# Kernel optimization log

Measured on AMD Instinct MI355X. Metric: run time of the kernel, lower is better.

## Reference

```python
import jax, jax.numpy as jnp
import numpy as np

NUM_HEADS = 16
LN_EPS = 1e-5


def setup_inputs() -> dict:
    key = jax.random.key(0)
    k1, k2, k3 = jax.random.split(key, 3)
    E = 1024
    B, S = 4, 2048
    return {
        "rotation_params": jax.random.normal(k1, (E, E), dtype=jnp.float32) * (E ** -0.5),
        "entangle_params": jax.random.normal(k2, (E, E), dtype=jnp.float32) * (E ** -0.5),
        "inputs": jax.random.normal(k3, (B, S, E), dtype=jnp.float32),
        "ln_weight": jnp.ones((E,), dtype=jnp.float32),
        "ln_bias": jnp.zeros((E,), dtype=jnp.float32),
    }


def reference(rotation_params, entangle_params, inputs, ln_weight, ln_bias):
    x = inputs  # (B, S, E)
    B, S, E = x.shape
    H = NUM_HEADS
    D = E // H
    scale = D ** -0.5

    q = jnp.einsum('bse,ef->bsf', x, rotation_params)
    k = jnp.einsum('bse,ef->bsf', x, entangle_params)
    v = x  # forward uses raw inputs as values

    # split heads: (B, H, S, D)
    q = q.reshape(B, S, H, D).transpose(0, 2, 1, 3)
    k = k.reshape(B, S, H, D).transpose(0, 2, 1, 3)
    v = v.reshape(B, S, H, D).transpose(0, 2, 1, 3)

    scores = jnp.einsum('bhsd,bhtd->bhst', q, k) * scale  # (B, H, S, S)
    attn = jax.nn.softmax(scores, axis=-1)
    context = jnp.einsum('bhst,bhtd->bhsd', attn, v)
    context = context.transpose(0, 2, 1, 3).reshape(B, S, E)

    # residual + LayerNorm
    y = context + x
    mu = jnp.mean(y, axis=-1, keepdims=True)
    var = jnp.mean(jnp.square(y - mu), axis=-1, keepdims=True)
    y = (y - mu) * jax.lax.rsqrt(var + LN_EPS)
    return y * ln_weight + ln_bias
```

## Files before the change

kernel.cpp:

```cpp
#include <hip/hip_runtime.h>
#include <hip/hip_bf16.h>

#define LOG2E 1.44269504088896340736f

typedef __attribute__((ext_vector_type(8)))  short  short8;
typedef __attribute__((ext_vector_type(2)))  float  f32x2;
typedef __attribute__((ext_vector_type(4)))  float  f32x4;
typedef __attribute__((ext_vector_type(16))) float  f32x16;

__device__ __forceinline__ unsigned short f2bf(float f) {
  unsigned u = __builtin_bit_cast(unsigned, f);
  return (unsigned short)((u + 0x8000u) >> 16);
}
__device__ __forceinline__ float bf2f(unsigned short u) {
  return __builtin_bit_cast(float, (unsigned)u << 16);
}
__device__ __forceinline__ f32x2 pkadd(f32x2 a, f32x2 b) {
  f32x2 r; asm("v_pk_add_f32 %0, %1, %2" : "=v"(r) : "v"(a), "v"(b)); return r;
}
__device__ __forceinline__ unsigned cvtpk2(float a, float b) {
  unsigned r; asm("v_cvt_pk_bf16_f32 %0, %1, %2" : "=v"(r) : "v"(a), "v"(b)); return r;
}
__device__ __forceinline__ float hexp2(float x) {
  float r; asm("v_exp_f32 %0, %1" : "=v"(r) : "v"(x)); return r;
}
__device__ __forceinline__ float m3(float a, float b, float c) {
  return fmaxf(fmaxf(a, b), c);
}
__device__ __forceinline__ void gl16(const void* g, void* l) {
  __builtin_amdgcn_global_load_lds(
      (const __attribute__((address_space(1))) void*)g,
      (__attribute__((address_space(3))) void*)l, 16, 0, 0);
}


__global__ __launch_bounds__(256) void prep_wt(const float* __restrict__ R,
                                               const float* __restrict__ En,
                                               unsigned short* __restrict__ Rt,
                                               unsigned short* __restrict__ Et) {
  const float* src = blockIdx.z ? En : R;
  unsigned short* dst = blockIdx.z ? Et : Rt;
  __shared__ unsigned short t[64][65];
  int e0 = blockIdx.y * 64, f0 = blockIdx.x * 64;
  int tid = threadIdx.x;
  int r = tid >> 2, c4 = (tid & 3) * 16;
#pragma unroll
  for (int j = 0; j < 16; j += 4) {
    float4 v = *(const float4*)(src + (size_t)(e0 + r) * 1024 + f0 + c4 + j);
    t[c4 + j + 0][r] = f2bf(v.x);
    t[c4 + j + 1][r] = f2bf(v.y);
    t[c4 + j + 2][r] = f2bf(v.z);
    t[c4 + j + 3][r] = f2bf(v.w);
  }
  __syncthreads();
  short8 o0, o1;
#pragma unroll
  for (int j = 0; j < 8; j++) {
    o0[j] = (short)t[r][c4 + j];
    o1[j] = (short)t[r][c4 + 8 + j];
  }
  *(short8*)(dst + (size_t)(f0 + r) * 1024 + e0 + c4) = o0;
  *(short8*)(dst + (size_t)(f0 + r) * 1024 + e0 + c4 + 8) = o1;
}

__global__ __launch_bounds__(256) void prep_vt(const float* __restrict__ x,
                                               unsigned short* __restrict__ vt,
                                               unsigned short* __restrict__ xb) {
  int bh = blockIdx.y, b = bh >> 4, h = bh & 15;
  int s0 = blockIdx.x * 64;
  __shared__ unsigned short t[64][65];
  int tid = threadIdx.x;
  int r = tid >> 2, c4 = (tid & 3) * 16;
#pragma unroll
  for (int j = 0; j < 16; j += 4) {
    float4 v = *(const float4*)(x + (size_t)(b * 2048 + s0 + r) * 1024 + h * 64 + c4 + j);
    ushort4 o;
    o.x = f2bf(v.x); o.y = f2bf(v.y); o.z = f2bf(v.z); o.w = f2bf(v.w);
    t[c4 + j + 0][r] = o.x;
    t[c4 + j + 1][r] = o.y;
    t[c4 + j + 2][r] = o.z;
    t[c4 + j + 3][r] = o.w;
    *(ushort4*)(xb + (size_t)(b * 2048 + s0 + r) * 1024 + h * 64 + c4 + j) = o;
  }
  __syncthreads();
  short8 o0, o1;
#pragma unroll
  for (int j = 0; j < 8; j++) {
    o0[j] = (short)t[r][c4 + j];
    o1[j] = (short)t[r][c4 + 8 + j];
  }
  *(short8*)(vt + (size_t)(bh * 64 + r) * 2048 + s0 + c4) = o0;
  *(short8*)(vt + (size_t)(bh * 64 + r) * 2048 + s0 + c4 + 8) = o1;
}

__global__ __launch_bounds__(256) void gemm_qk2(const unsigned short* __restrict__ A,
                                                const unsigned short* __restrict__ Bw,
                                                unsigned short* __restrict__ qb,
                                                unsigned short* __restrict__ kb,
                                                float qs) {
  int m0 = blockIdx.x * 128, n0 = blockIdx.y * 128;
  int tid = threadIdx.x;
  int w = tid >> 6, l = tid & 63;
  int wr = w >> 1, wc = w & 1;
  int l15 = l & 15, lq = l >> 4;

  __shared__ unsigned short As[128 * 64];
  __shared__ unsigned short Bs[128 * 64];

  f32x4 acc[4][4] = {};

  for (int k0 = 0; k0 < 1024; k0 += 64) {
    __syncthreads();
#pragma unroll
    for (int i = 0; i < 4; i++) {
      int row = i * 32 + (tid >> 3), ch = tid & 7;
      gl16(A  + (size_t)(m0 + row) * 1024 + k0 + ((ch ^ (row & 7)) << 3),
           (char*)As + i * 4096 + w * 1024);
      gl16(Bw + (size_t)(n0 + row) * 1024 + k0 + ((ch ^ (row & 7)) << 3),
           (char*)Bs + i * 4096 + w * 1024);
    }
    __syncthreads();

    short8 af[4][2], bfr[4][2];
#pragma unroll
    for (int mf = 0; mf < 4; mf++)
#pragma unroll
      for (int kk = 0; kk < 2; kk++) {
        int row = wr * 64 + mf * 16 + l15;
        int kb2 = (kk * 32 + lq * 8) * 2;
        af[mf][kk] = *(const short8*)((const char*)As + row * 128 + (kb2 ^ ((row & 7) << 4)));
      }
#pragma unroll
    for (int nf = 0; nf < 4; nf++)
#pragma unroll
      for (int kk = 0; kk < 2; kk++) {
        int row = wc * 64 + nf * 16 + l15;
        int kb2 = (kk * 32 + lq * 8) * 2;
        bfr[nf][kk] = *(const short8*)((const char*)Bs + row * 128 + (kb2 ^ ((row & 7) << 4)));
      }
#pragma unroll
    for (int mf = 0; mf < 4; mf++)
#pragma unroll
      for (int nf = 0; nf < 4; nf++)
#pragma unroll
        for (int kk = 0; kk < 2; kk++)
          acc[mf][nf] = __builtin_amdgcn_mfma_f32_16x16x32_bf16(
              af[mf][kk], bfr[nf][kk], acc[mf][nf], 0, 0, 0);
  }

  unsigned short* out = (n0 < 1024) ? qb : kb;
  float scale = (n0 < 1024) ? qs : 1.0f;
  int cb = n0 & 1023;
#pragma unroll
  for (int mf = 0; mf < 4; mf++)
#pragma unroll
    for (int nf = 0; nf < 4; nf++)
#pragma unroll
      for (int r = 0; r < 4; r++) {
        int grow = m0 + wr * 64 + mf * 16 + lq * 4 + r;
        int gcol = cb + wc * 64 + nf * 16 + l15;
        out[(size_t)grow * 1024 + gcol] = f2bf(acc[mf][nf][r] * scale);
      }
}

__global__ __launch_bounds__(256, 4) void attn_k(const unsigned short* __restrict__ Q,
                                                 const unsigned short* __restrict__ K,
                                                 const unsigned short* __restrict__ VT,
                                                 unsigned short* __restrict__ ctx) {
  int f = blockIdx.x;
  int bh = ((f >> 7) << 3) | (f & 7);
  int qt = (f >> 3) & 15;
  int b = bh >> 4, h = bh & 15;
  int q0 = qt * 128;
  int tid = threadIdx.x;
  int w = tid >> 6, l = tid & 63;
  int lh = l >> 5, l31 = l & 31;

  __shared__ unsigned short Kl[2 * 64 * 64];
  __shared__ unsigned short Vl[2 * 64 * 64];

  int qrow = q0 + w * 32 + l31;
  const unsigned short* qp = Q + (size_t)(b * 2048 + qrow) * 1024 + h * 64;
  short8 qf[4];
#pragma unroll
  for (int dk = 0; dk < 4; dk++) qf[dk] = *(const short8*)(qp + dk * 16 + lh * 8);

  int key = (l31 & 7) << 4;
  int koff[4], voff[4];
#pragma unroll
  for (int dk = 0; dk < 4; dk++) koff[dk] = l31 * 128 + ((dk * 32 + lh * 16) ^ key);
#pragma unroll
  for (int tf = 0; tf < 2; tf++)
#pragma unroll
    for (int kk = 0; kk < 2; kk++)
      voff[tf * 2 + kk] = l31 * 128 + ((tf * 64 + kk * 32 + lh * 16) ^ key);

  const char* KB = (const char*)Kl;
  const char* VB = (const char*)Vl;

  f32x16 cacc[2] = {};
  float mrun = -INFINITY, lsl = 0.f;

#define STAGE(buf, tt)                                                        \
  {                                                                           \
    _Pragma("unroll") for (int i_ = 0; i_ < 2; i_++) {                        \
      int row_ = i_ * 32 + (tid >> 3), ch_ = tid & 7;                         \
      gl16(K + (size_t)(b * 2048 + (tt) + row_) * 1024 + h * 64 +             \
               ((ch_ ^ (row_ & 7)) << 3),                                     \
           (char*)Kl + (buf) * 8192 + i_ * 4096 + w * 1024);                  \
      gl16(VT + (size_t)(bh * 64 + row_) * 2048 + (tt) +                      \
               ((ch_ ^ (row_ & 7)) << 3),                                     \
           (char*)Vl + (buf) * 8192 + i_ * 4096 + w * 1024);                  \
    }                                                                         \
  }

#define COMPUTE(IMM)                                                          \
  do {                                                                        \
    f32x16 sacc[2] = {};                                                      \
    __builtin_amdgcn_s_setprio(1);                                            \
    _Pragma("unroll") for (int tf = 0; tf < 2; tf++)                          \
      _Pragma("unroll") for (int dk = 0; dk < 4; dk++) {                      \
        short8 kf = *(const short8*)(KB + koff[dk] + (IMM) + tf * 4096);      \
        sacc[tf] = __builtin_amdgcn_mfma_f32_32x32x16_bf16(kf, qf[dk],        \
                                                           sacc[tf], 0, 0, 0);\
      }                                                                       \
    __builtin_amdgcn_s_setprio(0);                                            \
    float t16[16];                                                            \
    _Pragma("unroll") for (int j = 0; j < 16; j++)                            \
      t16[j] = fmaxf(sacc[0][j], sacc[1][j]);                                 \
    float t8[8];                                                              \
    _Pragma("unroll") for (int j = 0; j < 8; j++)                             \
      t8[j] = fmaxf(t16[j], t16[j + 8]);                                      \
    float lmax = m3(m3(t8[0], t8[1], t8[2]), m3(t8[3], t8[4], t8[5]),         \
                    fmaxf(t8[6], t8[7]));                                     \
    if (!__all(lmax <= mrun + 8.f)) {                                         \
      unsigned lu = __builtin_bit_cast(unsigned, lmax);                       \
      auto rr = __builtin_amdgcn_permlane32_swap(lu, lu, false, false);       \
      float pm = fmaxf(__builtin_bit_cast(float, rr[0]),                      \
                       __builtin_bit_cast(float, rr[1]));                     \
      float mnew = fmaxf(mrun, pm);                                           \
      float alpha = hexp2(mrun - mnew);                                       \
      mrun = mnew; lsl *= alpha;                                              \
      _Pragma("unroll") for (int r = 0; r < 16; r++) {                        \
        int rowq = (r & 3) + ((r >> 2) << 3) + (lh << 2);                     \
        float ar = __shfl(alpha, rowq, 64);                                   \
        cacc[0][r] *= ar; cacc[1][r] *= ar;                                   \
      }                                                                       \
    }                                                                         \
    f32x2 negm2; negm2[0] = -mrun; negm2[1] = -mrun;                          \
    f32x2 r2; r2[0] = 0.f; r2[1] = 0.f;                                       \
    _Pragma("unroll") for (int tf = 0; tf < 2; tf++) {                        \
      unsigned pw[8];                                                         \
      _Pragma("unroll") for (int j = 0; j < 8; j++) {                         \
        f32x2 s2; s2[0] = sacc[tf][2 * j]; s2[1] = sacc[tf][2 * j + 1];       \
        f32x2 d = pkadd(s2, negm2);                                           \
        float e0 = hexp2(d[0]), e1 = hexp2(d[1]);                             \
        f32x2 e2; e2[0] = e0; e2[1] = e1;                                     \
        r2 = pkadd(r2, e2);                                                   \
        pw[j] = cvtpk2(e0, e1);                                               \
      }                                                                       \
      short8 pa[2];                                                           \
      _Pragma("unroll") for (int kk = 0; kk < 2; kk++) {                      \
        auto r02 = __builtin_amdgcn_permlane32_swap(pw[kk * 4 + 0],           \
                                                    pw[kk * 4 + 2], false, false); \
        auto r13 = __builtin_amdgcn_permlane32_swap(pw[kk * 4 + 1],           \
                                                    pw[kk * 4 + 3], false, false); \
        union { unsigned u[4]; short8 s8; } wv;                               \
        wv.u[0] = r02[0]; wv.u[1] = r13[0];                                   \
        wv.u[2] = r02[1]; wv.u[3] = r13[1];                                   \
        pa[kk] = wv.s8;                                                       \
      }                                                                       \
      __builtin_amdgcn_s_setprio(1);                                          \
      _Pragma("unroll") for (int kk = 0; kk < 2; kk++)                        \
        _Pragma("unroll") for (int df = 0; df < 2; df++) {                    \
          short8 vf = *(const short8*)(VB + voff[tf * 2 + kk] + (IMM) +       \
                                       df * 4096);                            \
          cacc[df] = __builtin_amdgcn_mfma_f32_32x32x16_bf16(pa[kk], vf,      \
                                                             cacc[df], 0, 0, 0); \
        }                                                                     \
      __builtin_amdgcn_s_setprio(0);                                          \
    }                                                                         \
    lsl += r2[0] + r2[1];                                                     \
  } while (0)

  STAGE(0, 0);
  __syncthreads();

  for (int tc2 = 0; tc2 < 16; tc2++) {
    int t0 = tc2 * 128;
    STAGE(1, t0 + 64);
    COMPUTE(0);
    __syncthreads();
    if (tc2 < 15) STAGE(0, t0 + 128);
    COMPUTE(8192);
    __syncthreads();
  }
#undef STAGE
#undef COMPUTE

  {
    unsigned lu = __builtin_bit_cast(unsigned, lsl);
    auto rr = __builtin_amdgcn_permlane32_swap(lu, lu, false, false);
    lsl = __builtin_bit_cast(float, rr[0]) + __builtin_bit_cast(float, rr[1]);
  }
  float linv = 1.f / lsl;
#pragma unroll
  for (int r = 0; r < 16; r++) {
    int rowq = (r & 3) + ((r >> 2) << 3) + (lh << 2);
    float lr = __shfl(linv, rowq, 64);
    size_t base = (size_t)(b * 2048 + q0 + w * 32 + rowq) * 1024 + h * 64 + l31;
    ctx[base]      = f2bf(cacc[0][r] * lr);
    ctx[base + 32] = f2bf(cacc[1][r] * lr);
  }
}

__global__ __launch_bounds__(256) void ln_k(const unsigned short* __restrict__ ctx,
                                            const float* __restrict__ x,
                                            const float* __restrict__ wgt,
                                            const float* __restrict__ bgam,
                                            float* __restrict__ out) {
  int row = blockIdx.x;
  int tid = threadIdx.x;
  size_t base = (size_t)row * 1024 + tid * 4;
  ushort4 cu = *(const ushort4*)(ctx + base);
  float4 xv = *(const float4*)(x + base);
  float4 y;
  y.x = bf2f(cu.x) + xv.x; y.y = bf2f(cu.y) + xv.y;
  y.z = bf2f(cu.z) + xv.z; y.w = bf2f(cu.w) + xv.w;
  float s  = y.x + y.y + y.z + y.w;
  float ss = y.x * y.x + y.y * y.y + y.z * y.z + y.w * y.w;
#pragma unroll
  for (int o = 32; o >= 1; o >>= 1) {
    s  += __shfl_xor(s, o, 64);
    ss += __shfl_xor(ss, o, 64);
  }
  __shared__ float sm[8];
  if ((tid & 63) == 0) { sm[(tid >> 6) * 2] = s; sm[(tid >> 6) * 2 + 1] = ss; }
  __syncthreads();
  s  = sm[0] + sm[2] + sm[4] + sm[6];
  ss = sm[1] + sm[3] + sm[5] + sm[7];
  float mu = s * (1.f / 1024.f);
  float var = ss * (1.f / 1024.f) - mu * mu;
  float rstd = rsqrtf(var + 1e-5f);
  float4 wv = *(const float4*)(wgt + tid * 4);
  float4 bv = *(const float4*)(bgam + tid * 4);
  float4 o4;
  o4.x = (y.x - mu) * rstd * wv.x + bv.x;
  o4.y = (y.y - mu) * rstd * wv.y + bv.y;
  o4.z = (y.z - mu) * rstd * wv.z + bv.z;
  o4.w = (y.w - mu) * rstd * wv.w + bv.w;
  *(float4*)(out + base) = o4;
}

extern "C" void kernel_launch(void* const* d_in, const int* in_sizes, int n_in,
                              void* d_out, int out_size, void* d_ws, size_t ws_size,
                              hipStream_t stream) {
  (void)in_sizes; (void)n_in; (void)out_size; (void)ws_size;
  const float* R  = (const float*)d_in[0];
  const float* En = (const float*)d_in[1];
  const float* x  = (const float*)d_in[2];
  const float* lw = (const float*)d_in[3];
  const float* lb = (const float*)d_in[4];
  float* out = (float*)d_out;

  char* ws = (char*)d_ws;
  unsigned short* xb  = (unsigned short*)(ws);
  unsigned short* qb  = (unsigned short*)(ws + (size_t)(16u << 20));
  unsigned short* kb  = (unsigned short*)(ws + (size_t)(32u << 20));
  unsigned short* vt  = (unsigned short*)(ws + (size_t)(48u << 20));
  unsigned short* ctx = (unsigned short*)(ws + (size_t)(64u << 20));
  unsigned short* rt  = (unsigned short*)(ws + (size_t)(96u << 20));
  unsigned short* et  = (unsigned short*)(ws + (size_t)(98u << 20));

  prep_wt<<<dim3(16, 16, 2), 256, 0, stream>>>(R, En, rt, et);
  prep_vt<<<dim3(32, 64), 256, 0, stream>>>(x, vt, xb);
  gemm_qk2<<<dim3(64, 16), 256, 0, stream>>>(xb, rt, qb, kb, 0.125f * LOG2E);
  attn_k<<<1024, 256, 0, stream>>>(qb, kb, vt, ctx);
  ln_k<<<8192, 256, 0, stream>>>(ctx, x, lw, lb, out);
}
```

Baseline: 251.5 us.

## Rewrite QK projection GEMM as 256x256 double-buffered 8-wave pipelined kernel

Replaces the 128x128 single-buffered QK projection GEMM with a 256x256 tile kernel using 512 threads (8 waves). LDS is double-buffered, and the next k-tile's global loads are issued in quarters interleaved with MFMA phases under explicit barriers and raised wave priority. The intent is to hide global-to-LDS latency and raise operand reuse per loaded byte. In exchange it uses much more LDS and registers per block and launches only 256 blocks, which may leave some CUs underused.

New measurement: 243.9 us. 1.03x faster.

```diff
diff --git a/kernel.cpp b/kernel.cpp
--- a/kernel.cpp
+++ b/kernel.cpp
@@ -93,71 +93,128 @@
   *(short8*)(vt + (size_t)(bh * 64 + r) * 2048 + s0 + c4 + 8) = o1;
 }
 
-__global__ __launch_bounds__(256) void gemm_qk2(const unsigned short* __restrict__ A,
+__global__ __launch_bounds__(512, 2) void gemm8(const unsigned short* __restrict__ A,
                                                 const unsigned short* __restrict__ Bw,
                                                 unsigned short* __restrict__ qb,
                                                 unsigned short* __restrict__ kb,
                                                 float qs) {
-  int m0 = blockIdx.x * 128, n0 = blockIdx.y * 128;
+  int m0 = blockIdx.x * 256;
+  int by = blockIdx.y;
+  int n0 = by * 256;
   int tid = threadIdx.x;
   int w = tid >> 6, l = tid & 63;
-  int wr = w >> 1, wc = w & 1;
+  int wr = w >> 2, wc = w & 3;
   int l15 = l & 15, lq = l >> 4;
 
-  __shared__ unsigned short As[128 * 64];
-  __shared__ unsigned short Bs[128 * 64];
-
-  f32x4 acc[4][4] = {};
-
-  for (int k0 = 0; k0 < 1024; k0 += 64) {
-    __syncthreads();
-#pragma unroll
-    for (int i = 0; i < 4; i++) {
-      int row = i * 32 + (tid >> 3), ch = tid & 7;
-      gl16(A  + (size_t)(m0 + row) * 1024 + k0 + ((ch ^ (row & 7)) << 3),
-           (char*)As + i * 4096 + w * 1024);
-      gl16(Bw + (size_t)(n0 + row) * 1024 + k0 + ((ch ^ (row & 7)) << 3),
-           (char*)Bs + i * 4096 + w * 1024);
+  __shared__ unsigned short As[2][2][128 * 64];
+  __shared__ unsigned short Bs[2][2][128 * 64];
+
+  f32x4 acc[8][4] = {};
+
+  int key = (l15 & 7) << 4;
+  const char* pA[2];
+  const char* pB[2];
+#pragma unroll
+  for (int kk = 0; kk < 2; kk++) {
+    pA[kk] = (const char*)As + wr * 16384 + l15 * 128 + ((kk * 64 + lq * 16) ^ key);
+    pB[kk] = (const char*)Bs + (wc >> 1) * 16384 + ((wc & 1) * 64 + l15) * 128 +
+             ((kk * 64 + lq * 16) ^ key);
+  }
+
+#define SHALF(buf, kt, which)                                                 \
+  do {                                                                        \
+    const unsigned short* src_ = ((which) < 2)                                \
+        ? (A  + (size_t)(m0 + ((which) & 1) * 128) * 1024)                    \
+        : (Bw + (size_t)(n0 + ((which) & 1) * 128) * 1024);                   \
+    char* dst_ = (char*)(((which) < 2) ? &As[buf][(which) & 1][0]             \
+                                       : &Bs[buf][(which) & 1][0]);           \
+    int k0_ = (kt) * 64;                                                      \
+    _Pragma("unroll") for (int i_ = 0; i_ < 2; i_++) {                        \
+      int flat_ = i_ * 512 + tid;                                             \
+      int row_ = flat_ >> 3, ch_ = flat_ & 7;                                 \
+      gl16(src_ + (size_t)row_ * 1024 + k0_ + ((ch_ ^ (row_ & 7)) << 3),      \
+           dst_ + i_ * 8192 + w * 1024);                                      \
+    }                                                                         \
+  } while (0)
+
+#define BARX()                                                                \
+  do {                                                                        \
+    __builtin_amdgcn_sched_barrier(0);                                        \
+    asm volatile("" ::: "memory");                                            \
+    __builtin_amdgcn_s_barrier();                                             \
+    asm volatile("" ::: "memory");                                            \
+    __builtin_amdgcn_sched_barrier(0);                                        \
+  } while (0)
+
+#define DSRD(buf, mq, nq)                                                     \
+  short8 af[4][2]; short8 bfv[2][2];                                          \
+  _Pragma("unroll") for (int mfq = 0; mfq < 4; mfq++)                         \
+    _Pragma("unroll") for (int kk = 0; kk < 2; kk++)                          \
+      af[mfq][kk] = *(const short8*)(pA[kk] + (buf) * 32768 + (mq) * 8192 +   \
+                                     mfq * 2048);                             \
+  _Pragma("unroll") for (int nfq = 0; nfq < 2; nfq++)                         \
+    _Pragma("unroll") for (int kk = 0; kk < 2; kk++)                          \
+      bfv[nfq][kk] = *(const short8*)(pB[kk] + (buf) * 32768 + (nq) * 4096 +  \
+                                      nfq * 2048);
+
+#define MM(mq, nq)                                                            \
+  asm volatile("s_waitcnt lgkmcnt(0)" ::: "memory");                          \
+  __builtin_amdgcn_sched_barrier(0);                                          \
+  __builtin_amdgcn_s_setprio(1);                                              \
+  _Pragma("unroll") for (int mfq = 0; mfq < 4; mfq++)                         \
+    _Pragma("unroll") for (int nfq = 0; nfq < 2; nfq++)                       \
+      _Pragma("unroll") for (int kk = 0; kk < 2; kk++)                        \
+        acc[(mq) * 4 + mfq][(nq) * 2 + nfq] =                                 \
+            __builtin_amdgcn_mfma_f32_16x16x32_bf16(                          \
+                af[mfq][kk], bfv[nfq][kk],                                    \
+                acc[(mq) * 4 + mfq][(nq) * 2 + nfq], 0, 0, 0);                \
+  __builtin_amdgcn_s_setprio(0);
+
+  SHALF(0, 0, 0); SHALF(0, 0, 1); SHALF(0, 0, 2); SHALF(0, 0, 3);
+  asm volatile("s_waitcnt vmcnt(0)" ::: "memory");
+  BARX();
+
+  for (int kt = 0; kt < 16; kt++) {
+    int buf = kt & 1, nb = buf ^ 1;
+    {
+      DSRD(buf, 0, 0);
+      if (kt < 15) { SHALF(nb, kt + 1, 0); SHALF(nb, kt + 1, 1); }
+      MM(0, 0);
+      BARX();
     }
-    __syncthreads();
-
-    short8 af[4][2], bfr[4][2];
-#pragma unroll
-    for (int mf = 0; mf < 4; mf++)
-#pragma unroll
-      for (int kk = 0; kk < 2; kk++) {
-        int row = wr * 64 + mf * 16 + l15;
-        int kb2 = (kk * 32 + lq * 8) * 2;
-        af[mf][kk] = *(const short8*)((const char*)As + row * 128 + (kb2 ^ ((row & 7) << 4)));
-      }
+    {
+      DSRD(buf, 0, 1);
+      if (kt < 15) { SHALF(nb, kt + 1, 2); SHALF(nb, kt + 1, 3); }
+      MM(0, 1);
+      BARX();
+    }
+    {
+      DSRD(buf, 1, 0);
+      MM(1, 0);
+      BARX();
+    }
+    {
+      DSRD(buf, 1, 1);
+      MM(1, 1);
+      asm volatile("s_waitcnt vmcnt(0)" ::: "memory");
+      BARX();
+    }
+  }
+#undef SHALF
+#undef DSRD
+#undef MM
+#undef BARX
+
+  unsigned short* out = (by < 4) ? qb : kb;
+  float scale = (by < 4) ? qs : 1.0f;
+  int cb = (by & 3) * 256;
+#pragma unroll
+  for (int mf = 0; mf < 8; mf++)
 #pragma unroll
     for (int nf = 0; nf < 4; nf++)
 #pragma unroll
-      for (int kk = 0; kk < 2; kk++) {
-        int row = wc * 64 + nf * 16 + l15;
-        int kb2 = (kk * 32 + lq * 8) * 2;
-        bfr[nf][kk] = *(const short8*)((const char*)Bs + row * 128 + (kb2 ^ ((row & 7) << 4)));
-      }
-#pragma unroll
-    for (int mf = 0; mf < 4; mf++)
-#pragma unroll
-      for (int nf = 0; nf < 4; nf++)
-#pragma unroll
-        for (int kk = 0; kk < 2; kk++)
-          acc[mf][nf] = __builtin_amdgcn_mfma_f32_16x16x32_bf16(
-              af[mf][kk], bfr[nf][kk], acc[mf][nf], 0, 0, 0);
-  }
-
-  unsigned short* out = (n0 < 1024) ? qb : kb;
-  float scale = (n0 < 1024) ? qs : 1.0f;
-  int cb = n0 & 1023;
-#pragma unroll
-  for (int mf = 0; mf < 4; mf++)
-#pragma unroll
-    for (int nf = 0; nf < 4; nf++)
-#pragma unroll
       for (int r = 0; r < 4; r++) {
-        int grow = m0 + wr * 64 + mf * 16 + lq * 4 + r;
+        int grow = m0 + wr * 128 + mf * 16 + lq * 4 + r;
         int gcol = cb + wc * 64 + nf * 16 + l15;
         out[(size_t)grow * 1024 + gcol] = f2bf(acc[mf][nf][r] * scale);
       }
@@ -374,7 +431,7 @@
 
   prep_wt<<<dim3(16, 16, 2), 256, 0, stream>>>(R, En, rt, et);
   prep_vt<<<dim3(32, 64), 256, 0, stream>>>(x, vt, xb);
-  gemm_qk2<<<dim3(64, 16), 256, 0, stream>>>(xb, rt, qb, kb, 0.125f * LOG2E);
+  gemm8<<<dim3(32, 8), 512, 0, stream>>>(xb, rt, qb, kb, 0.125f * LOG2E);
   attn_k<<<1024, 256, 0, stream>>>(qb, kb, vt, ctx);
   ln_k<<<8192, 256, 0, stream>>>(ctx, x, lw, lb, out);
 }
```
